# Kernel optimization log

Measured on AMD Instinct MI355X. Metric: run time of the kernel, lower is better.

The kernel has to match this reference:

```python
import jax, jax.numpy as jnp
import numpy as np

B, T, D, H = 512, 128, 128, 2048  # batch, seq_len, input/output dim, hidden dim
W_SCALE = 0.02


def setup_inputs() -> dict:
    key = jax.random.key(0)
    ks = jax.random.split(key, 4)
    return {
        "tgt": jax.random.normal(ks[0], (B, T, D), jnp.float32),
        "W_ih": jax.random.normal(ks[1], (4 * H, D), jnp.float32) * W_SCALE,
        "W_hh": jax.random.normal(ks[2], (4 * H, H), jnp.float32) * W_SCALE,
        "b_ih": jnp.zeros((4 * H,), jnp.float32),
        "b_hh": jnp.zeros((4 * H,), jnp.float32),
        "W_out": jax.random.normal(ks[3], (D, H), jnp.float32) * W_SCALE,
        "b_out": jnp.zeros((D,), jnp.float32),
    }


def reference(tgt, W_ih, W_hh, b_ih, b_hh, W_out, b_out):
    # LSTMDecoder.forward with teacher_forcing_ratio=0.0 (deterministic,
    # tgt: [B, T, D]; first frame tgt[:, 0] seeds the decoder.
    batch, max_len, _ = tgt.shape
    hidden = W_hh.shape[1]
    b = b_ih + b_hh  # fuse the two LSTM biases

    def step(carry, _):
        x, h, c = carry
        # torch nn.LSTM gate order: i, f, g, o
        gates = x @ W_ih.T + h @ W_hh.T + b  # [B, 4H]
        i, f, g, o = jnp.split(gates, 4, axis=-1)
        c = jax.nn.sigmoid(f) * c + jax.nn.sigmoid(i) * jnp.tanh(g)
        h = jax.nn.sigmoid(o) * jnp.tanh(c)
        out = h @ W_out.T + b_out  # [B, D]
        return (out, h, c), out

    h0 = jnp.zeros((batch, hidden), tgt.dtype)
    c0 = jnp.zeros((batch, hidden), tgt.dtype)
    _, outs = jax.lax.scan(step, (tgt[:, 0, :], h0, c0), None, length=max_len)
    return outs.transpose(1, 0, 2)  # [B, T, D]
```

## Files before the change

kernel.cpp:

```cpp
#include <hip/hip_runtime.h>
#include <hip/hip_fp16.h>

typedef _Float16 f16;
typedef __attribute__((ext_vector_type(8))) _Float16 f16x8;
typedef __attribute__((ext_vector_type(4))) float f32x4;

__device__ __forceinline__ void gemm_core(
    const f16* __restrict__ A, int lda,
    const f16* __restrict__ Bm, int ldb,
    int K, int bm0, int nbase, int nstride,
    f16* As, f16* Bs, f32x4 acc[2][4])
{
    const int tid  = threadIdx.x;
    const int wave = tid >> 6;
    const int lane = tid & 63;
    const int l15  = lane & 15;
    const int quad = lane >> 4;

    #pragma unroll
    for (int mt = 0; mt < 2; ++mt)
      #pragma unroll
      for (int nt = 0; nt < 4; ++nt)
        acc[mt][nt] = (f32x4){0.f, 0.f, 0.f, 0.f};

    const f16* gA[4];
    #pragma unroll
    for (int p = 0; p < 4; ++p) {
        int s = p * 256 + tid;
        int r = s >> 3;
        int cg = (s & 7) ^ (r & 7);
        gA[p] = A + (size_t)(bm0 + r) * lda + cg * 8;
    }
    const f16* gB[2];
    #pragma unroll
    for (int p = 0; p < 2; ++p) {
        int s = p * 256 + tid;
        int r = s >> 3;
        int cg = (s & 7) ^ (r & 7);
        int brow = nbase + (r >> 4) * nstride + (r & 15);
        gB[p] = Bm + (size_t)brow * ldb + cg * 8;
    }
    f16* ldsA[4];
    #pragma unroll
    for (int p = 0; p < 4; ++p) ldsA[p] = As + (p * 256 + wave * 64) * 8;
    f16* ldsB[2];
    #pragma unroll
    for (int p = 0; p < 2; ++p) ldsB[p] = Bs + (p * 256 + wave * 64) * 8;

    auto stage = [&](int buf, int k0) {
        #pragma unroll
        for (int p = 0; p < 4; ++p)
            __builtin_amdgcn_global_load_lds(
                (const __attribute__((address_space(1))) void*)(gA[p] + k0),
                (__attribute__((address_space(3))) void*)(ldsA[p] + buf * 8192),
                16, 0, 0);
        #pragma unroll
        for (int p = 0; p < 2; ++p)
            __builtin_amdgcn_global_load_lds(
                (const __attribute__((address_space(1))) void*)(gB[p] + k0),
                (__attribute__((address_space(3))) void*)(ldsB[p] + buf * 4096),
                16, 0, 0);
    };

    int offA[2][2], offB[4][2];
    #pragma unroll
    for (int mt = 0; mt < 2; ++mt) {
        int r = wave * 32 + mt * 16 + l15;
        #pragma unroll
        for (int kk = 0; kk < 2; ++kk)
            offA[mt][kk] = (r * 8 + (((kk << 2) | quad) ^ (r & 7))) * 8;
    }
    #pragma unroll
    for (int nt = 0; nt < 4; ++nt) {
        int r = nt * 16 + l15;
        #pragma unroll
        for (int kk = 0; kk < 2; ++kk)
            offB[nt][kk] = (r * 8 + (((kk << 2) | quad) ^ (r & 7))) * 8;
    }

    const int niter = K >> 6;
    stage(0, 0);
    stage(1, 64);
    for (int t = 0; t < niter; ++t) {
        if (t + 1 < niter)
            asm volatile("s_waitcnt vmcnt(6)" ::: "memory");
        else
            asm volatile("s_waitcnt vmcnt(0)" ::: "memory");
        __builtin_amdgcn_s_barrier();
        const f16* Ab = As + (t & 1) * 8192;
        const f16* Bb = Bs + (t & 1) * 4096;
        f16x8 af[2][2], bf[4][2];
        #pragma unroll
        for (int mt = 0; mt < 2; ++mt)
          #pragma unroll
          for (int kk = 0; kk < 2; ++kk)
            af[mt][kk] = *(const f16x8*)(Ab + offA[mt][kk]);
        #pragma unroll
        for (int nt = 0; nt < 4; ++nt)
          #pragma unroll
          for (int kk = 0; kk < 2; ++kk)
            bf[nt][kk] = *(const f16x8*)(Bb + offB[nt][kk]);
        asm volatile("s_waitcnt lgkmcnt(0)" ::: "memory");
        __builtin_amdgcn_s_barrier();
        if (t + 2 < niter) stage(t & 1, (t + 2) << 6);
        #pragma unroll
        for (int kk = 0; kk < 2; ++kk)
          #pragma unroll
          for (int mt = 0; mt < 2; ++mt)
            #pragma unroll
            for (int nt = 0; nt < 4; ++nt)
              acc[mt][nt] = __builtin_amdgcn_mfma_f32_16x16x32_f16(
                  af[mt][kk], bf[nt][kk], acc[mt][nt], 0, 0, 0);
    }
}

__global__ __launch_bounds__(256, 2) void k_step(
    const f16* __restrict__ A, int lda, int K,
    const f16* __restrict__ W, int ldb,
    const float* __restrict__ bias,
    float* __restrict__ Cst,
    f16* __restrict__ Hout)
{
    __shared__ alignas(16) f16 As[16384];
    __shared__ alignas(16) f16 Bs[8192];
    const int hid0 = blockIdx.x * 16;
    const int bm0  = blockIdx.y * 128;
    f32x4 acc[2][4];
    gemm_core(A, lda, W, ldb, K, bm0, hid0, 2048, As, Bs, acc);

    const int lane = threadIdx.x & 63;
    const int wave = threadIdx.x >> 6;
    const int l15 = lane & 15, quad = lane >> 4;
    const int hid = hid0 + l15;
    const float bI = bias[hid];
    const float bF = bias[2048 + hid];
    const float bG = bias[4096 + hid];
    const float bO = bias[6144 + hid];
    #pragma unroll
    for (int mt = 0; mt < 2; ++mt) {
      #pragma unroll
      for (int reg = 0; reg < 4; ++reg) {
        const int row = bm0 + wave * 32 + mt * 16 + quad * 4 + reg;
        const size_t idx = (size_t)row * 2048 + hid;
        float iv = acc[mt][0][reg] + bI;
        float fv = acc[mt][1][reg] + bF;
        float gv = acc[mt][2][reg] + bG;
        float ov = acc[mt][3][reg] + bO;
        float si = 1.f / (1.f + __expf(-iv));
        float sf = 1.f / (1.f + __expf(-fv));
        float so = 1.f / (1.f + __expf(-ov));
        float tg = tanhf(gv);
        float c = sf * Cst[idx] + si * tg;
        Cst[idx] = c;
        Hout[idx] = (f16)(so * tanhf(c));
      }
    }
}

__global__ __launch_bounds__(256, 2) void k_out(
    const f16* __restrict__ Hbase,
    const f16* __restrict__ Wout,
    const float* __restrict__ bout,
    float* __restrict__ out, int t0)
{
    __shared__ alignas(16) f16 As[16384];
    __shared__ alignas(16) f16 Bs[8192];
    const int ng  = blockIdx.x;
    const int bm0 = blockIdx.y * 128;
    f32x4 acc[2][4];
    gemm_core(Hbase, 2048, Wout, 2048, 2048, bm0, ng * 64, 16, As, Bs, acc);
    const int lane = threadIdx.x & 63;
    const int wave = threadIdx.x >> 6;
    const int l15 = lane & 15, quad = lane >> 4;
    #pragma unroll
    for (int mt = 0; mt < 2; ++mt) {
      #pragma unroll
      for (int nt = 0; nt < 4; ++nt) {
        const int d = ng * 64 + nt * 16 + l15;
        const float bo = bout[d];
        #pragma unroll
        for (int reg = 0; reg < 4; ++reg) {
          const int m = bm0 + wave * 32 + mt * 16 + quad * 4 + reg;
          const int slot = m >> 9, b = m & 511;
          const int t = t0 + slot;
          out[(size_t)b * 16384 + t * 128 + d] = acc[mt][nt][reg] + bo;
        }
      }
    }
}


__global__ void k_cast(const float* __restrict__ s, f16* __restrict__ d, int n)
{
    int i = blockIdx.x * 256 + threadIdx.x;
    if (i < n) d[i] = (f16)s[i];
}

__global__ void k_x0(const float* __restrict__ tgt, f16* __restrict__ x0)
{
    int i = blockIdx.x * 256 + threadIdx.x;
    int b = i >> 7, d = i & 127;
    x0[i] = (f16)tgt[(size_t)b * 16384 + d];
}

__global__ void k_bias(const float* __restrict__ bih, const float* __restrict__ bhh,
                       const float* __restrict__ Wih, const float* __restrict__ bout,
                       float* __restrict__ b0, float* __restrict__ bp)
{
    int r = blockIdx.x * 256 + threadIdx.x;
    if (r >= 8192) return;
    float s = bih[r] + bhh[r];
    float a = 0.f;
    for (int d = 0; d < 128; ++d) a += Wih[(size_t)r * 128 + d] * bout[d];
    b0[r] = s;
    bp[r] = s + a;
}

__global__ void k_wt(const float* __restrict__ Wout, f16* __restrict__ WoutT)
{
    __shared__ float tile[64][65];
    const int k0 = blockIdx.x * 64;
    const int d0 = blockIdx.y * 64;
    const int tid = threadIdx.x;
    const int c = tid & 63, rr = tid >> 6;
    #pragma unroll
    for (int i = 0; i < 16; ++i) {
        int d = rr + i * 4;
        tile[d][c] = Wout[(size_t)(d0 + d) * 2048 + k0 + c];
    }
    __syncthreads();
    #pragma unroll
    for (int i = 0; i < 16; ++i) {
        int k = rr + i * 4;
        WoutT[(size_t)(k0 + k) * 128 + d0 + c] = (f16)tile[c][k];
    }
}

__global__ __launch_bounds__(256, 2) void k_wcomb2(
    const f16* __restrict__ Wih16, const f16* __restrict__ WoutT,
    const float* __restrict__ Whh, f16* __restrict__ Wc)
{
    __shared__ alignas(16) f16 As[16384];
    __shared__ alignas(16) f16 Bs[8192];
    const int n0  = blockIdx.x * 64;
    const int bm0 = blockIdx.y * 128;
    f32x4 acc[2][4];
    gemm_core(Wih16, 128, WoutT, 128, 128, bm0, n0, 16, As, Bs, acc);
    const int lane = threadIdx.x & 63;
    const int wave = threadIdx.x >> 6;
    const int l15 = lane & 15, quad = lane >> 4;
    #pragma unroll
    for (int mt = 0; mt < 2; ++mt) {
      #pragma unroll
      for (int nt = 0; nt < 4; ++nt) {
        const int k = n0 + nt * 16 + l15;
        #pragma unroll
        for (int reg = 0; reg < 4; ++reg) {
          const int r = bm0 + wave * 32 + mt * 16 + quad * 4 + reg;
          Wc[(size_t)r * 2048 + k] =
              (f16)(acc[mt][nt][reg] + Whh[(size_t)r * 2048 + k]);
        }
      }
    }
}


extern "C" void kernel_launch(void* const* d_in, const int* in_sizes, int n_in,
                              void* d_out, int out_size, void* d_ws, size_t ws_size,
                              hipStream_t stream)
{
    const float* tgt  = (const float*)d_in[0];
    const float* Wih  = (const float*)d_in[1];
    const float* Whh  = (const float*)d_in[2];
    const float* bih  = (const float*)d_in[3];
    const float* bhh  = (const float*)d_in[4];
    const float* Wout = (const float*)d_in[5];
    const float* bout = (const float*)d_in[6];
    float* out = (float*)d_out;

    char* ws = (char*)d_ws;
    size_t off = 0;
    auto alloc = [&](size_t bytes) -> void* {
        void* p = ws + off;
        off += (bytes + 255) & ~(size_t)255;
        return p;
    };
    f16*   Wc     = (f16*)alloc((size_t)8192 * 2048 * 2);
    f16*   Wih16  = (f16*)alloc((size_t)8192 * 128 * 2);
    f16*   Wout16 = (f16*)alloc((size_t)128 * 2048 * 2);
    f16*   WoutT  = (f16*)alloc((size_t)2048 * 128 * 2);
    f16*   x0     = (f16*)alloc((size_t)512 * 128 * 2);
    float* b0     = (float*)alloc(8192 * 4);
    float* bp     = (float*)alloc(8192 * 4);
    float* Cst    = (float*)alloc((size_t)512 * 2048 * 4);

    const size_t slotsz = (size_t)512 * 2048;
    int depth = 0;
    const int cands[7] = {128, 64, 32, 16, 8, 4, 2};
    for (int i = 0; i < 7; ++i)
        if (off + (size_t)cands[i] * slotsz * 2 <= ws_size) { depth = cands[i]; break; }
    if (depth == 0) return;
    f16* Hbuf = (f16*)alloc((size_t)depth * slotsz * 2);

    hipMemsetAsync(Cst, 0, (size_t)512 * 2048 * 4, stream);
    k_cast<<<dim3(4096), dim3(256), 0, stream>>>(Wih, Wih16, 1048576);
    k_cast<<<dim3(1024), dim3(256), 0, stream>>>(Wout, Wout16, 262144);
    k_wt<<<dim3(32, 2), dim3(256), 0, stream>>>(Wout, WoutT);
    k_x0<<<dim3(256), dim3(256), 0, stream>>>(tgt, x0);
    k_bias<<<dim3(32), dim3(256), 0, stream>>>(bih, bhh, Wih, bout, b0, bp);
    k_wcomb2<<<dim3(32, 64), dim3(256), 0, stream>>>(Wih16, WoutT, Whh, Wc);

    k_step<<<dim3(128, 4), dim3(256), 0, stream>>>(x0, 128, 128, Wih16, 128, b0, Cst, Hbuf);
    for (int s = 1; s < 128; ++s) {
        if ((s % depth) == 0)
            k_out<<<dim3(2, depth * 4), dim3(256), 0, stream>>>(Hbuf, Wout16, bout, out, s - depth);
        k_step<<<dim3(128, 4), dim3(256), 0, stream>>>(
            Hbuf + (size_t)((s - 1) % depth) * slotsz, 2048, 2048, Wc, 2048, bp,
            Cst, Hbuf + (size_t)(s % depth) * slotsz);
    }
    k_out<<<dim3(2, depth * 4), dim3(256), 0, stream>>>(Hbuf, Wout16, bout, out, 128 - depth);
}
```

Measured before the change: 3.824 ms.

## Switch GEMM core to 128x128 tiles with 32x32x16 MFMA and LDS-staged gate epilogue

The shared GEMM core now uses a 128x128 block tile split 2x2 across waves and issues 32x32x16 f16 MFMAs instead of 16x16x32. It double-buffers register fragments across two LDS stages. The step kernel covers 32 hidden units across all four gates per block, so the grid shrinks from 512 to 256 blocks, and the gate epilogue goes through an LDS transpose. Larger tiles reuse more data per load. The costs are lower occupancy (launch bounds 1), fewer blocks than CUs on the per-step kernel, and an extra LDS round trip in the epilogue.

```diff
diff --git a/kernel.cpp b/kernel.cpp
--- a/kernel.cpp
+++ b/kernel.cpp
@@ -3,190 +3,215 @@
 
 typedef _Float16 f16;
 typedef __attribute__((ext_vector_type(8))) _Float16 f16x8;
-typedef __attribute__((ext_vector_type(4))) float f32x4;
+typedef __attribute__((ext_vector_type(16))) float f32x16;
+
+#define GLL(src, dst) __builtin_amdgcn_global_load_lds( \
+    (const __attribute__((address_space(1))) void*)(src), \
+    (__attribute__((address_space(3))) void*)(dst), 16, 0, 0)
 
 __device__ __forceinline__ void gemm_core(
     const f16* __restrict__ A, int lda,
     const f16* __restrict__ Bm, int ldb,
     int K, int bm0, int nbase, int nstride,
-    f16* As, f16* Bs, f32x4 acc[2][4])
+    unsigned char* __restrict__ smem, f32x16 acc[2][2])
 {
     const int tid  = threadIdx.x;
     const int wave = tid >> 6;
+    const int wr   = wave >> 1;
+    const int wc   = wave & 1;
     const int lane = tid & 63;
-    const int l15  = lane & 15;
-    const int quad = lane >> 4;
+    const int l31  = lane & 31;
+    const int hi   = lane >> 5;
 
     #pragma unroll
     for (int mt = 0; mt < 2; ++mt)
       #pragma unroll
-      for (int nt = 0; nt < 4; ++nt)
-        acc[mt][nt] = (f32x4){0.f, 0.f, 0.f, 0.f};
-
-    const f16* gA[4];
+      for (int nt = 0; nt < 2; ++nt)
+        #pragma unroll
+        for (int e = 0; e < 16; ++e)
+          acc[mt][nt][e] = 0.f;
+
+    const f16* gA[4]; const f16* gB[4];
+    int ldA[4], ldB[4];
     #pragma unroll
     for (int p = 0; p < 4; ++p) {
-        int s = p * 256 + tid;
-        int r = s >> 3;
+        int s  = p * 256 + tid;
+        int r  = s >> 3;
         int cg = (s & 7) ^ (r & 7);
         gA[p] = A + (size_t)(bm0 + r) * lda + cg * 8;
-    }
-    const f16* gB[2];
-    #pragma unroll
-    for (int p = 0; p < 2; ++p) {
-        int s = p * 256 + tid;
-        int r = s >> 3;
-        int cg = (s & 7) ^ (r & 7);
-        int brow = nbase + (r >> 4) * nstride + (r & 15);
+        int brow = nbase + (r >> 5) * nstride + (r & 31);
         gB[p] = Bm + (size_t)brow * ldb + cg * 8;
-    }
-    f16* ldsA[4];
-    #pragma unroll
-    for (int p = 0; p < 4; ++p) ldsA[p] = As + (p * 256 + wave * 64) * 8;
-    f16* ldsB[2];
-    #pragma unroll
-    for (int p = 0; p < 2; ++p) ldsB[p] = Bs + (p * 256 + wave * 64) * 8;
-
-    auto stage = [&](int buf, int k0) {
-        #pragma unroll
-        for (int p = 0; p < 4; ++p)
-            __builtin_amdgcn_global_load_lds(
-                (const __attribute__((address_space(1))) void*)(gA[p] + k0),
-                (__attribute__((address_space(3))) void*)(ldsA[p] + buf * 8192),
-                16, 0, 0);
-        #pragma unroll
-        for (int p = 0; p < 2; ++p)
-            __builtin_amdgcn_global_load_lds(
-                (const __attribute__((address_space(1))) void*)(gB[p] + k0),
-                (__attribute__((address_space(3))) void*)(ldsB[p] + buf * 4096),
-                16, 0, 0);
+        ldA[p] = (p * 256 + wave * 64) * 16;
+        ldB[p] = 16384 + (p * 256 + wave * 64) * 16;
+    }
+
+    int offA[2][4], offB[2][4];
+    #pragma unroll
+    for (int mt = 0; mt < 2; ++mt) {
+        int ra = wr * 64 + mt * 32 + l31;
+        #pragma unroll
+        for (int kk = 0; kk < 4; ++kk)
+            offA[mt][kk] = (ra * 8 + ((kk * 2 + hi) ^ (ra & 7))) * 8;
+    }
+    #pragma unroll
+    for (int nt = 0; nt < 2; ++nt) {
+        int rb = wc * 64 + nt * 32 + l31;
+        #pragma unroll
+        for (int kk = 0; kk < 4; ++kk)
+            offB[nt][kk] = 8192 + (rb * 8 + ((kk * 2 + hi) ^ (rb & 7))) * 8;
+    }
+
+    auto stage = [&](int buf, int t2) {
+        unsigned char* base = smem + buf * 32768;
+        const int k0 = t2 * 64;
+        #pragma unroll
+        for (int p = 0; p < 4; ++p) GLL(gA[p] + k0, base + ldA[p]);
+        #pragma unroll
+        for (int p = 0; p < 4; ++p) GLL(gB[p] + k0, base + ldB[p]);
     };
-
-    int offA[2][2], offB[4][2];
-    #pragma unroll
-    for (int mt = 0; mt < 2; ++mt) {
-        int r = wave * 32 + mt * 16 + l15;
-        #pragma unroll
-        for (int kk = 0; kk < 2; ++kk)
-            offA[mt][kk] = (r * 8 + (((kk << 2) | quad) ^ (r & 7))) * 8;
-    }
-    #pragma unroll
-    for (int nt = 0; nt < 4; ++nt) {
-        int r = nt * 16 + l15;
-        #pragma unroll
-        for (int kk = 0; kk < 2; ++kk)
-            offB[nt][kk] = (r * 8 + (((kk << 2) | quad) ^ (r & 7))) * 8;
-    }
-
-    const int niter = K >> 6;
-    stage(0, 0);
-    stage(1, 64);
-    for (int t = 0; t < niter; ++t) {
-        if (t + 1 < niter)
-            asm volatile("s_waitcnt vmcnt(6)" ::: "memory");
-        else
-            asm volatile("s_waitcnt vmcnt(0)" ::: "memory");
-        __builtin_amdgcn_s_barrier();
-        const f16* Ab = As + (t & 1) * 8192;
-        const f16* Bb = Bs + (t & 1) * 4096;
-        f16x8 af[2][2], bf[4][2];
+    auto rdfr = [&](int buf, f16x8 (&af)[2][4], f16x8 (&bf)[2][4]) {
+        const f16* base = (const f16*)(smem + buf * 32768);
         #pragma unroll
         for (int mt = 0; mt < 2; ++mt)
           #pragma unroll
-          for (int kk = 0; kk < 2; ++kk)
-            af[mt][kk] = *(const f16x8*)(Ab + offA[mt][kk]);
-        #pragma unroll
-        for (int nt = 0; nt < 4; ++nt)
+          for (int kk = 0; kk < 4; ++kk)
+            af[mt][kk] = *(const f16x8*)(base + offA[mt][kk]);
+        #pragma unroll
+        for (int nt = 0; nt < 2; ++nt)
           #pragma unroll
-          for (int kk = 0; kk < 2; ++kk)
-            bf[nt][kk] = *(const f16x8*)(Bb + offB[nt][kk]);
-        asm volatile("s_waitcnt lgkmcnt(0)" ::: "memory");
-        __builtin_amdgcn_s_barrier();
-        if (t + 2 < niter) stage(t & 1, (t + 2) << 6);
-        #pragma unroll
-        for (int kk = 0; kk < 2; ++kk)
+          for (int kk = 0; kk < 4; ++kk)
+            bf[nt][kk] = *(const f16x8*)(base + offB[nt][kk]);
+    };
+    auto mm = [&](f16x8 (&af)[2][4], f16x8 (&bf)[2][4]) {
+        #pragma unroll
+        for (int kk = 0; kk < 4; ++kk)
           #pragma unroll
           for (int mt = 0; mt < 2; ++mt)
             #pragma unroll
-            for (int nt = 0; nt < 4; ++nt)
-              acc[mt][nt] = __builtin_amdgcn_mfma_f32_16x16x32_f16(
+            for (int nt = 0; nt < 2; ++nt)
+              acc[mt][nt] = __builtin_amdgcn_mfma_f32_32x32x16_f16(
                   af[mt][kk], bf[nt][kk], acc[mt][nt], 0, 0, 0);
-    }
-}
-
-__global__ __launch_bounds__(256, 2) void k_step(
+    };
+
+    const int niter = K >> 6;
+    f16x8 aX[2][4], bX[2][4], aY[2][4], bY[2][4];
+    stage(0, 0);
+    stage(1, 1);
+    asm volatile("s_waitcnt vmcnt(8)" ::: "memory");
+    __builtin_amdgcn_s_barrier();
+    __builtin_amdgcn_sched_barrier(0);
+    rdfr(0, aX, bX);
+
+    for (int t = 0; t < niter; t += 2) {
+        asm volatile("s_waitcnt lgkmcnt(0)" ::: "memory");
+        __builtin_amdgcn_sched_barrier(0);
+        __builtin_amdgcn_s_barrier();
+        __builtin_amdgcn_sched_barrier(0);
+        if (t + 2 < niter) stage(0, t + 2);
+        if (t + 2 < niter) asm volatile("s_waitcnt vmcnt(8)" ::: "memory");
+        else               asm volatile("s_waitcnt vmcnt(0)" ::: "memory");
+        __builtin_amdgcn_s_barrier();
+        __builtin_amdgcn_sched_barrier(0);
+        rdfr(1, aY, bY);
+        mm(aX, bX);
+        asm volatile("s_waitcnt lgkmcnt(0)" ::: "memory");
+        __builtin_amdgcn_sched_barrier(0);
+        __builtin_amdgcn_s_barrier();
+        __builtin_amdgcn_sched_barrier(0);
+        if (t + 3 < niter) stage(1, t + 3);
+        if (t + 2 < niter) {
+            if (t + 3 < niter) asm volatile("s_waitcnt vmcnt(8)" ::: "memory");
+            else               asm volatile("s_waitcnt vmcnt(0)" ::: "memory");
+            __builtin_amdgcn_s_barrier();
+            __builtin_amdgcn_sched_barrier(0);
+            rdfr(0, aX, bX);
+        }
+        mm(aY, bY);
+    }
+}
+
+__global__ __launch_bounds__(256, 1) void k_step(
     const f16* __restrict__ A, int lda, int K,
     const f16* __restrict__ W, int ldb,
     const float* __restrict__ bias,
     float* __restrict__ Cst,
     f16* __restrict__ Hout)
 {
-    __shared__ alignas(16) f16 As[16384];
-    __shared__ alignas(16) f16 Bs[8192];
-    const int hid0 = blockIdx.x * 16;
+    __shared__ alignas(16) unsigned char smem[65536];
+    const int hid0 = blockIdx.x * 32;
     const int bm0  = blockIdx.y * 128;
-    f32x4 acc[2][4];
-    gemm_core(A, lda, W, ldb, K, bm0, hid0, 2048, As, Bs, acc);
-
-    const int lane = threadIdx.x & 63;
-    const int wave = threadIdx.x >> 6;
-    const int l15 = lane & 15, quad = lane >> 4;
-    const int hid = hid0 + l15;
+    f32x16 acc[2][2];
+    gemm_core(A, lda, W, ldb, K, bm0, hid0, 2048, smem, acc);
+
+    const int tid = threadIdx.x;
+    const int wave = tid >> 6, wr = wave >> 1, wc = wave & 1;
+    const int lane = tid & 63, l31 = lane & 31, hi = lane >> 5;
+    float* G = (float*)smem;
+    #pragma unroll
+    for (int mt = 0; mt < 2; ++mt)
+      #pragma unroll
+      for (int nt = 0; nt < 2; ++nt) {
+        const int col = wc * 64 + nt * 32 + l31;
+        #pragma unroll
+        for (int reg = 0; reg < 16; ++reg) {
+          const int row = wr * 64 + mt * 32 + (reg & 3) + 8 * (reg >> 2) + 4 * hi;
+          G[row * 128 + col] = acc[mt][nt][reg];
+        }
+      }
+    __syncthreads();
+    const int hl  = tid & 31;
+    const int r8  = tid >> 5;
+    const int hid = hid0 + hl;
     const float bI = bias[hid];
     const float bF = bias[2048 + hid];
     const float bG = bias[4096 + hid];
     const float bO = bias[6144 + hid];
     #pragma unroll
-    for (int mt = 0; mt < 2; ++mt) {
-      #pragma unroll
-      for (int reg = 0; reg < 4; ++reg) {
-        const int row = bm0 + wave * 32 + mt * 16 + quad * 4 + reg;
-        const size_t idx = (size_t)row * 2048 + hid;
-        float iv = acc[mt][0][reg] + bI;
-        float fv = acc[mt][1][reg] + bF;
-        float gv = acc[mt][2][reg] + bG;
-        float ov = acc[mt][3][reg] + bO;
+    for (int j = 0; j < 16; ++j) {
+        const int row = j * 8 + r8;
+        const float* g = G + row * 128;
+        float iv = g[hl]      + bI;
+        float fv = g[32 + hl] + bF;
+        float gv = g[64 + hl] + bG;
+        float ov = g[96 + hl] + bO;
         float si = 1.f / (1.f + __expf(-iv));
         float sf = 1.f / (1.f + __expf(-fv));
         float so = 1.f / (1.f + __expf(-ov));
         float tg = tanhf(gv);
+        const size_t idx = (size_t)(bm0 + row) * 2048 + hid;
         float c = sf * Cst[idx] + si * tg;
         Cst[idx] = c;
         Hout[idx] = (f16)(so * tanhf(c));
-      }
-    }
-}
-
-__global__ __launch_bounds__(256, 2) void k_out(
+    }
+}
+
+__global__ __launch_bounds__(256, 1) void k_out(
     const f16* __restrict__ Hbase,
     const f16* __restrict__ Wout,
     const float* __restrict__ bout,
     float* __restrict__ out, int t0)
 {
-    __shared__ alignas(16) f16 As[16384];
-    __shared__ alignas(16) f16 Bs[8192];
-    const int ng  = blockIdx.x;
+    __shared__ alignas(16) unsigned char smem[65536];
     const int bm0 = blockIdx.y * 128;
-    f32x4 acc[2][4];
-    gemm_core(Hbase, 2048, Wout, 2048, 2048, bm0, ng * 64, 16, As, Bs, acc);
-    const int lane = threadIdx.x & 63;
-    const int wave = threadIdx.x >> 6;
-    const int l15 = lane & 15, quad = lane >> 4;
-    #pragma unroll
-    for (int mt = 0; mt < 2; ++mt) {
+    f32x16 acc[2][2];
+    gemm_core(Hbase, 2048, Wout, 2048, 2048, bm0, 0, 32, smem, acc);
+    const int tid = threadIdx.x;
+    const int wave = tid >> 6, wr = wave >> 1, wc = wave & 1;
+    const int lane = tid & 63, l31 = lane & 31, hi = lane >> 5;
+    #pragma unroll
+    for (int mt = 0; mt < 2; ++mt)
       #pragma unroll
-      for (int nt = 0; nt < 4; ++nt) {
-        const int d = ng * 64 + nt * 16 + l15;
+      for (int nt = 0; nt < 2; ++nt) {
+        const int d = wc * 64 + nt * 32 + l31;
         const float bo = bout[d];
         #pragma unroll
-        for (int reg = 0; reg < 4; ++reg) {
-          const int m = bm0 + wave * 32 + mt * 16 + quad * 4 + reg;
+        for (int reg = 0; reg < 16; ++reg) {
+          const int row = wr * 64 + mt * 32 + (reg & 3) + 8 * (reg >> 2) + 4 * hi;
+          const int m = bm0 + row;
           const int slot = m >> 9, b = m & 511;
-          const int t = t0 + slot;
-          out[(size_t)b * 16384 + t * 128 + d] = acc[mt][nt][reg] + bo;
+          out[(size_t)b * 16384 + (t0 + slot) * 128 + d] = acc[mt][nt][reg] + bo;
         }
       }
-    }
 }
 
 
@@ -236,32 +261,30 @@
     }
 }
 
-__global__ __launch_bounds__(256, 2) void k_wcomb2(
+__global__ __launch_bounds__(256, 1) void k_wcomb2(
     const f16* __restrict__ Wih16, const f16* __restrict__ WoutT,
     const float* __restrict__ Whh, f16* __restrict__ Wc)
 {
-    __shared__ alignas(16) f16 As[16384];
-    __shared__ alignas(16) f16 Bs[8192];
-    const int n0  = blockIdx.x * 64;
+    __shared__ alignas(16) unsigned char smem[65536];
+    const int n0  = blockIdx.x * 128;
     const int bm0 = blockIdx.y * 128;
-    f32x4 acc[2][4];
-    gemm_core(Wih16, 128, WoutT, 128, 128, bm0, n0, 16, As, Bs, acc);
-    const int lane = threadIdx.x & 63;
-    const int wave = threadIdx.x >> 6;
-    const int l15 = lane & 15, quad = lane >> 4;
-    #pragma unroll
-    for (int mt = 0; mt < 2; ++mt) {
+    f32x16 acc[2][2];
+    gemm_core(Wih16, 128, WoutT, 128, 128, bm0, n0, 32, smem, acc);
+    const int tid = threadIdx.x;
+    const int wave = tid >> 6, wr = wave >> 1, wc = wave & 1;
+    const int lane = tid & 63, l31 = lane & 31, hi = lane >> 5;
+    #pragma unroll
+    for (int mt = 0; mt < 2; ++mt)
       #pragma unroll
-      for (int nt = 0; nt < 4; ++nt) {
-        const int k = n0 + nt * 16 + l15;
-        #pragma unroll
-        for (int reg = 0; reg < 4; ++reg) {
-          const int r = bm0 + wave * 32 + mt * 16 + quad * 4 + reg;
-          Wc[(size_t)r * 2048 + k] =
-              (f16)(acc[mt][nt][reg] + Whh[(size_t)r * 2048 + k]);
+      for (int nt = 0; nt < 2; ++nt) {
+        const int k = n0 + wc * 64 + nt * 32 + l31;
+        #pragma unroll
+        for (int reg = 0; reg < 16; ++reg) {
+          const int row = wr * 64 + mt * 32 + (reg & 3) + 8 * (reg >> 2) + 4 * hi;
+          const size_t r = (size_t)(bm0 + row);
+          Wc[r * 2048 + k] = (f16)(acc[mt][nt][reg] + Whh[r * 2048 + k]);
         }
       }
-    }
 }
 
 
@@ -308,15 +331,15 @@
     k_wt<<<dim3(32, 2), dim3(256), 0, stream>>>(Wout, WoutT);
     k_x0<<<dim3(256), dim3(256), 0, stream>>>(tgt, x0);
     k_bias<<<dim3(32), dim3(256), 0, stream>>>(bih, bhh, Wih, bout, b0, bp);
-    k_wcomb2<<<dim3(32, 64), dim3(256), 0, stream>>>(Wih16, WoutT, Whh, Wc);
-
-    k_step<<<dim3(128, 4), dim3(256), 0, stream>>>(x0, 128, 128, Wih16, 128, b0, Cst, Hbuf);
+    k_wcomb2<<<dim3(16, 64), dim3(256), 0, stream>>>(Wih16, WoutT, Whh, Wc);
+
+    k_step<<<dim3(64, 4), dim3(256), 0, stream>>>(x0, 128, 128, Wih16, 128, b0, Cst, Hbuf);
     for (int s = 1; s < 128; ++s) {
         if ((s % depth) == 0)
-            k_out<<<dim3(2, depth * 4), dim3(256), 0, stream>>>(Hbuf, Wout16, bout, out, s - depth);
-        k_step<<<dim3(128, 4), dim3(256), 0, stream>>>(
+            k_out<<<dim3(1, depth * 4), dim3(256), 0, stream>>>(Hbuf, Wout16, bout, out, s - depth);
+        k_step<<<dim3(64, 4), dim3(256), 0, stream>>>(
             Hbuf + (size_t)((s - 1) % depth) * slotsz, 2048, 2048, Wc, 2048, bp,
             Cst, Hbuf + (size_t)(s % depth) * slotsz);
     }
-    k_out<<<dim3(2, depth * 4), dim3(256), 0, stream>>>(Hbuf, Wout16, bout, out, 128 - depth);
-}
+    k_out<<<dim3(1, depth * 4), dim3(256), 0, stream>>>(Hbuf, Wout16, bout, out, 128 - depth);
+}
```

New measurement: 4.307 ms. +12.6%, slower.
